# Kernel optimization log

Hardware: AMD Instinct MI355X
Metric: run time of the kernel (lower is better)

The kernel has to match this reference:

```python
import jax, jax.numpy as jnp
import numpy as np

HEADS = 8
HIDDEN = 512
SEQ = 1024
BATCH = 8
SCALE = 1.2
TOPK = round(0.05 * SEQ)  # 51, as in mode='stocastic'


def setup_inputs() -> dict:
    key = jax.random.key(0)
    ks = jax.random.split(key, 12)
    d = HIDDEN
    s = 0.02
    return {
        "Query_x": jax.random.normal(ks[0], (BATCH, SEQ, d), jnp.float32),
        "KeyandValue_x": jax.random.normal(ks[1], (BATCH, SEQ, d), jnp.float32),
        "Wq": jax.random.normal(ks[2], (d, d), jnp.float32) * s,
        "bq": jnp.zeros((d,), jnp.float32),
        "Wk": jax.random.normal(ks[3], (d, d), jnp.float32) * s,
        "bk": jnp.zeros((d,), jnp.float32),
        "Wv": jax.random.normal(ks[4], (d, d), jnp.float32) * s,
        "bv": jnp.zeros((d,), jnp.float32),
        "Wo": jax.random.normal(ks[5], (d, d), jnp.float32) * s,
        "bo": jnp.zeros((d,), jnp.float32),
        "randidx": jax.random.randint(ks[6], (round(0.1 * SEQ),), 0, SEQ, jnp.int32),
    }


def _split_heads(x, B, S):
    # torch: split last dim into heads chunks, cat along dim 0 -> [heads*B, S, dk]
    dk = HIDDEN // HEADS
    return x.reshape(B, S, HEADS, dk).transpose(2, 0, 1, 3).reshape(HEADS * B, S, dk)


def _merge_heads(x, B, S):
    dk = HIDDEN // HEADS
    return x.reshape(HEADS, B, S, dk).transpose(1, 2, 0, 3).reshape(B, S, HIDDEN)


def moderate_attention(a, randidx):
    # a: [N, S, L] softmaxed attention. Scale top-k + random columns by SCALE,
    # then renormalize rows. torch scatter_ writes a*SCALE gathered from the
    # pre-scatter tensor, so duplicate indices are idempotent -> boolean mask.
    N, S, L = a.shape
    _, idx = jax.lax.top_k(a, TOPK)                       # [N, S, k]
    rand_b = jnp.broadcast_to(randidx.astype(idx.dtype), (N, S, randidx.shape[0]))
    all_idx = jnp.concatenate([idx, rand_b], axis=-1)      # [N, S, k+r]
    n_ix = jnp.arange(N)[:, None, None]
    q_ix = jnp.arange(S)[None, :, None]
    sel = jnp.zeros(a.shape, bool).at[n_ix, q_ix, all_idx].set(True)
    a2 = jnp.where(sel, a * SCALE, a)
    return a2 / jnp.sum(a2, axis=-1, keepdims=True)


def reference(Query_x, KeyandValue_x, Wq, bq, Wk, bk, Wv, bv, Wo, bo, randidx):
    B, S, _ = Query_x.shape
    dk = HIDDEN // HEADS
    Q = _split_heads(Query_x @ Wq + bq, B, S)          # [H*B, S, dk]
    K = _split_heads(KeyandValue_x @ Wk + bk, B, S)
    V = _split_heads(KeyandValue_x @ Wv + bv, B, S)
    scores = jnp.einsum('nqd,nkd->nqk', Q, K) / jnp.sqrt(jnp.float32(dk))
    a = jax.nn.softmax(scores, axis=-1)
    a = moderate_attention(a, randidx)
    out = jnp.einsum('nqk,nkd->nqd', a, V)
    return _merge_heads(out, B, S) @ Wo + bo
```

## Files before the change

kernel.cpp:

```cpp
#include <hip/hip_runtime.h>
#include <stdint.h>

typedef unsigned short ushort_t;
typedef __bf16 bf16x8 __attribute__((ext_vector_type(8)));
typedef _Float16 f16x8v __attribute__((ext_vector_type(8)));
typedef __fp16 fp16x2 __attribute__((ext_vector_type(2)));
typedef float f32x4 __attribute__((ext_vector_type(4)));

#define SEQ   1024
#define DK    64
#define TOPK_N 51
#define RSCALE 1.2f
#define LOG2E    1.44269504089f
#define LOG2_12  0.26303440583f

#define OFF_WT  0
#define OFF_Q   (4*512*512)
#define OFF_K   (OFF_Q  + 64*1024*64)
#define OFF_V   (OFF_K  + 64*1024*64)
#define OFF_QX  (OFF_V  + 64*1024*64)
#define OFF_KVX (OFF_QX + 8192*512)
#define OFF_MASK (OFF_KVX + 8192*512)
#define OFF_A   OFF_QX

static __device__ __forceinline__ ushort_t f2bf(float f){
  union { float f; unsigned u; } x; x.f = f;
  unsigned r = x.u + 0x7FFFu + ((x.u >> 16) & 1u);
  return (ushort_t)(r >> 16);
}
static __device__ __forceinline__ ushort_t f2h(float f){
  union { _Float16 h; ushort_t u; } x; x.h = (_Float16)f; return x.u;
}
static __device__ __forceinline__ float h2f(ushort_t u){
  union { ushort_t u; _Float16 h; } x; x.u = u; return (float)x.h;
}
static __device__ __forceinline__ unsigned pk2(float a, float b){
  union { fp16x2 h; unsigned u; } x;
  x.h = __builtin_amdgcn_cvt_pkrtz(a, b);
  return x.u;
}
static __device__ __forceinline__ unsigned pkrne(float a, float b){
  return (unsigned)f2h(a) | ((unsigned)f2h(b) << 16);
}
static __device__ __forceinline__ bf16x8 frag16(const ushort_t* p){
  union { uint4 u; bf16x8 b; } x; x.u = *(const uint4*)p; return x.b;
}
static __device__ __forceinline__ f16x8v frag16h(const ushort_t* p){
  union { uint4 u; f16x8v h; } x; x.u = *(const uint4*)p; return x.h;
}
static __device__ __forceinline__ void gll16(const ushort_t* g, ushort_t* lds){
  __builtin_amdgcn_global_load_lds((const __attribute__((address_space(1))) unsigned*)g,
                                   (__attribute__((address_space(3))) unsigned*)lds,
                                   16, 0, 0);
}

__global__ __launch_bounds__(256) void prep_k(const float* qx, const float* kvx,
    const float* Wq, const float* Wk, const float* Wv, const float* Wo,
    const int* ridx, int nrand, ushort_t* ws){
  __shared__ ushort_t t[64][72];
  __shared__ unsigned wds[64];
  int bid = blockIdx.x, tid = threadIdx.x;

  if (bid < 4096){
    const float* src = (bid >= 2048) ? kvx : qx;
    ushort_t* dst = ws + ((bid >= 2048) ? OFF_KVX : OFF_QX);
    int i = ((bid & 2047)*256 + tid) * 8;
    float4 a = *(const float4*)(src + i);
    float4 b = *(const float4*)(src + i + 4);
    union { ushort_t s[8]; uint4 u; } p;
    p.s[0]=f2bf(a.x); p.s[1]=f2bf(a.y); p.s[2]=f2bf(a.z); p.s[3]=f2bf(a.w);
    p.s[4]=f2bf(b.x); p.s[5]=f2bf(b.y); p.s[6]=f2bf(b.z); p.s[7]=f2bf(b.w);
    *(uint4*)(dst + i) = p.u;
  } else if (bid < 4352){
    int rb = bid - 4096;
    int z = rb >> 6, rem = rb & 63;
    const float* W = z==0?Wq: z==1?Wk: z==2?Wv: Wo;
    ushort_t* O = ws + OFF_WT + (size_t)z*512*512;
    int kt = (rem >> 3)*64, nt = (rem & 7)*64;
    int r0 = tid>>3, c8 = (tid&7)*8;
    #pragma unroll
    for (int p=0;p<2;p++){
      int r = p*32 + r0;
      float4 a = *(const float4*)&W[(size_t)(kt+r)*512 + nt + c8];
      float4 b = *(const float4*)&W[(size_t)(kt+r)*512 + nt + c8 + 4];
      t[r][c8+0]=f2bf(a.x); t[r][c8+1]=f2bf(a.y); t[r][c8+2]=f2bf(a.z); t[r][c8+3]=f2bf(a.w);
      t[r][c8+4]=f2bf(b.x); t[r][c8+5]=f2bf(b.y); t[r][c8+6]=f2bf(b.z); t[r][c8+7]=f2bf(b.w);
    }
    __syncthreads();
    #pragma unroll
    for (int p=0;p<2;p++){
      int r = p*32 + r0;
      union { ushort_t s[8]; uint4 u; } tmp;
      #pragma unroll
      for (int j=0;j<8;j++) tmp.s[j] = t[c8+j][r];
      *(uint4*)&O[(size_t)(nt+r)*512 + kt + c8] = tmp.u;
    }
  } else {
    if (tid < 64) wds[tid] = 0;
    __syncthreads();
    for (int i = tid; i < nrand; i += 256){
      int col = ridx[i];
      atomicOr(&wds[(col >> 3) & 63], 1u << (((col >> 9) << 3) | (col & 7)));
    }
    __syncthreads();
    if (tid < 64) (ws + OFF_MASK)[tid] = (ushort_t)wds[tid];
  }
}

__global__ __launch_bounds__(256) void gemm_k(ushort_t* ws, const float* bq, const float* bk,
    const float* bv, const float* bo, float* dout, int base_mode){
  int mode = base_mode + blockIdx.z;
  const ushort_t* X  = (mode==0)? ws+OFF_QX : (mode==3)? ws+OFF_A : ws+OFF_KVX;
  const ushort_t* WT = ws + OFF_WT + (size_t)mode*(512*512);
  const float* bias  = (mode==0)?bq:(mode==1)?bk:(mode==2)?bv:bo;
  ushort_t* out = (mode==0)? ws+OFF_Q : (mode==1)? ws+OFF_K : ws+OFF_V;

  __shared__ ushort_t sA[128*64];
  __shared__ ushort_t sB[128*64];
  int tid = threadIdx.x, lane = tid & 63, w = tid >> 6;
  int wm = w & 1, wn = w >> 1;
  int m0 = blockIdx.y * 128, n0 = blockIdx.x * 128;
  int r16 = lane & 15, quad = lane >> 4;
  int srow = lane >> 3, schunk = lane & 7;

  const f32x4 zero = {0.f,0.f,0.f,0.f};
  f32x4 acc[4][4];
  #pragma unroll
  for (int i=0;i<4;i++)
    #pragma unroll
    for (int j=0;j<4;j++) acc[i][j] = zero;

  for (int kb = 0; kb < 8; kb++){
    int k0 = kb*64;
    #pragma unroll
    for (int i=0;i<4;i++){
      int rb = w*32 + i*8;
      int gch = schunk ^ srow;
      gll16(X  + (size_t)(m0+rb+srow)*512 + k0 + gch*8, sA + rb*64);
      gll16(WT + (size_t)(n0+rb+srow)*512 + k0 + gch*8, sB + rb*64);
    }
    __syncthreads();
    #pragma unroll
    for (int t=0;t<2;t++){
      bf16x8 aF[4], bF[4];
      #pragma unroll
      for (int i=0;i<4;i++){
        int row = wm*64 + i*16 + r16;
        aF[i] = frag16(sA + row*64 + ((t*4 + quad) ^ (row & 7))*8);
      }
      #pragma unroll
      for (int j=0;j<4;j++){
        int row = wn*64 + j*16 + r16;
        bF[j] = frag16(sB + row*64 + ((t*4 + quad) ^ (row & 7))*8);
      }
      #pragma unroll
      for (int i=0;i<4;i++)
        #pragma unroll
        for (int j=0;j<4;j++)
          acc[i][j] = __builtin_amdgcn_mfma_f32_16x16x32_bf16(aF[i], bF[j], acc[i][j], 0,0,0);
    }
    __syncthreads();
  }

  #pragma unroll
  for (int i=0;i<4;i++){
    int rowbase = m0 + wm*64 + i*16 + quad*4;
    #pragma unroll
    for (int j=0;j<4;j++){
      int col = n0 + wn*64 + j*16 + r16;
      float bsv = bias[col];
      if (mode == 3){
        #pragma unroll
        for (int r=0;r<4;r++)
          dout[(size_t)(rowbase+r)*512 + col] = acc[i][j][r] + bsv;
      } else if (mode == 2){
        int b = rowbase >> 10, s = rowbase & 1023;
        int h = col >> 6, d = col & 63;
        int nh = h*8 + b;
        union { ushort_t sh[4]; uint2 u2; } pk;
        #pragma unroll
        for (int r=0;r<4;r++) pk.sh[r] = f2h(acc[i][j][r] + bsv);
        *(uint2*)&out[ (((size_t)nh*128 + (s>>3))*64 + d)*8 + (s&4) ] = pk.u2;
      } else if (mode == 1){
        int b = rowbase >> 10;
        int h = col >> 6, d = col & 63;
        int nh = h*8 + b;
        size_t base = (size_t)nh*65536 + (size_t)(d>>3)*8192 + (d&7);
        #pragma unroll
        for (int r=0;r<4;r++){
          int s = (rowbase + r) & 1023;
          out[ base + (size_t)s*8 ] = f2bf(acc[i][j][r] + bsv);
        }
      } else {
        int h = col >> 6, d = col & 63;
        #pragma unroll
        for (int r=0;r<4;r++){
          int row = rowbase + r;
          int b = row >> 10, s = row & 1023;
          int nh = h*8 + b;
          out[ ((size_t)nh*1024 + s)*64 + d ] = f2bf((acc[i][j][r] + bsv)*0.125f);
        }
      }
    }
  }
}

__global__ __launch_bounds__(256, 4) void attn_k(const ushort_t* ws_q, const ushort_t* ws_k,
     const ushort_t* ws_v, const ushort_t* maskp, ushort_t* attn){
  __shared__ __align__(16) ushort_t sS[16*1024];

  int tid = threadIdx.x, lane = tid&63, w = tid>>6;
  int r16 = lane&15, quad = lane>>4;
  int gid = blockIdx.x;
  int n  = (gid & 7)*8 + ((gid >> 3) >> 6);
  int q0 = ((gid >> 3) & 63) * 16;
  const ushort_t* Qn = ws_q + (size_t)n*SEQ*DK;
  const ushort_t* Kn = ws_k + (size_t)n*SEQ*DK;
  const ushort_t* Vb = ws_v + (size_t)n*SEQ*DK;

  unsigned rmask = (unsigned)maskp[lane];

  bf16x8 aQ[2];
  #pragma unroll
  for (int t=0;t<2;t++)
    aQ[t] = frag16(Qn + (size_t)(q0 + r16)*64 + t*32 + quad*8);

  const f32x4 zero = {0.f,0.f,0.f,0.f};

  #pragma unroll
  for (int half=0; half<2; half++){
    f32x4 acc[8];
    #pragma unroll
    for (int i=0;i<8;i++) acc[i] = zero;
    #pragma unroll
    for (int grp=0; grp<2; grp++){
      int c = half*2 + grp;
      bf16x8 bF[8];
      #pragma unroll
      for (int u=0;u<4;u++){
        int key = c*256 + w*64 + u*16 + r16;
        bF[u*2+0] = frag16(Kn + ((size_t)(quad    )*1024 + key)*8);
        bF[u*2+1] = frag16(Kn + ((size_t)(4 + quad)*1024 + key)*8);
      }
      __builtin_amdgcn_s_setprio(1);
      #pragma unroll
      for (int u=0;u<4;u++){
        int t8 = grp*4 + u;
        acc[t8] = __builtin_amdgcn_mfma_f32_16x16x32_bf16(bF[u*2+0], aQ[0], acc[t8], 0,0,0);
        acc[t8] = __builtin_amdgcn_mfma_f32_16x16x32_bf16(bF[u*2+1], aQ[1], acc[t8], 0,0,0);
      }
      __builtin_amdgcn_s_setprio(0);
    }
    int rs = r16 & 7;
    #pragma unroll
    for (int grp=0; grp<2; grp++)
      #pragma unroll
      for (int u=0;u<4;u++){
        int kb = (half*2+grp)*256 + w*64 + u*16 + quad*4;
        f32x4 a = acc[grp*4+u];
        uint2 o;
        o.x = pkrne(a[0], a[1]);
        o.y = pkrne(a[2], a[3]);
        *(uint2*)(sS + r16*1024 + (((kb>>3) ^ rs) << 3) + (kb & 4)) = o;
      }
  }
  __syncthreads();

  float v[4][16];
  float vmax[4];
  #pragma unroll
  for (int r=0;r<4;r++){
    int row = w*4 + r, rs = row & 7;
    const ushort_t* bp = sS + row*1024 + ((lane ^ rs) * 8);
    uint4 lo4 = *(const uint4*)bp;
    uint4 hi4 = *(const uint4*)(bp + 512);
    unsigned wl[8] = {lo4.x, lo4.y, lo4.z, lo4.w, hi4.x, hi4.y, hi4.z, hi4.w};
    float m = -3.0e38f;
    #pragma unroll
    for (int k=0;k<8;k++){
      float a = h2f((ushort_t)(wl[k] & 0xffffu));
      float b = h2f((ushort_t)(wl[k] >> 16));
      v[r][2*k] = a; v[r][2*k+1] = b;
      m = fmaxf(m, fmaxf(a, b));
    }
    vmax[r] = m;
  }
  #pragma unroll
  for (int r=0;r<4;r++)
    #pragma unroll
    for (int j=0;j<16;j++)
      asm volatile("" : "+v"(v[r][j]));

  #pragma unroll
  for (int off=32; off>=1; off>>=1)
    #pragma unroll
    for (int r=0;r<4;r++) vmax[r] = fmaxf(vmax[r], __shfl_xor(vmax[r], off));

  float blo[4], bhi[4];
  #pragma unroll
  for (int r=0;r<4;r++){ bhi[r] = vmax[r]; blo[r] = vmax[r] - 4.0f; }
  #pragma unroll 1
  for (int it=0; it<11; it++){
    #pragma unroll
    for (int r=0;r<4;r++){
      float mid = 0.5f*(blo[r]+bhi[r]);
      int cnt = 0;
      #pragma unroll
      for (int j=0;j<16;j++)
        cnt += __popcll(__ballot(v[r][j] >= mid));
      bool ge = (cnt >= TOPK_N);
      blo[r] = ge ? mid : blo[r];
      bhi[r] = ge ? bhi[r] : mid;
    }
  }
  float fb[16];
  #pragma unroll
  for (int j=0;j<16;j++) fb[j] = ((rmask >> j) & 1u) ? LOG2_12 : 0.0f;
  float sC = LOG2_12;
  asm volatile("" : "+v"(sC));

  float ls[4];
  #pragma unroll
  for (int r=0;r<4;r++){
    float thr = blo[r], s = 0.f;
    #pragma unroll
    for (int j=0;j<16;j++){
      float tb = (v[r][j] >= thr) ? sC : fb[j];
      float e = __builtin_amdgcn_exp2f(
                  __builtin_fmaf(v[r][j] - vmax[r], LOG2E, tb));
      v[r][j] = e; s += e;
    }
    ls[r] = s;
  }
  #pragma unroll
  for (int off=32; off>=1; off>>=1)
    #pragma unroll
    for (int r=0;r<4;r++) ls[r] += __shfl_xor(ls[r], off);
  #pragma unroll
  for (int r=0;r<4;r++){
    int row = w*4 + r, rs = row & 7;
    float rinv = 1.0f / ls[r];
    ushort_t* bp = sS + row*1024 + ((lane ^ rs) * 8);
    uint4 o0, o1;
    o0.x = pk2(v[r][0]*rinv,  v[r][1]*rinv);
    o0.y = pk2(v[r][2]*rinv,  v[r][3]*rinv);
    o0.z = pk2(v[r][4]*rinv,  v[r][5]*rinv);
    o0.w = pk2(v[r][6]*rinv,  v[r][7]*rinv);
    o1.x = pk2(v[r][8]*rinv,  v[r][9]*rinv);
    o1.y = pk2(v[r][10]*rinv, v[r][11]*rinv);
    o1.z = pk2(v[r][12]*rinv, v[r][13]*rinv);
    o1.w = pk2(v[r][14]*rinv, v[r][15]*rinv);
    *(uint4*)bp = o0;
    *(uint4*)(bp + 512) = o1;
  }
  __syncthreads();

  f32x4 oa0 = zero, oa1 = zero;
  int dd = w*16 + r16;
  #pragma unroll
  for (int kb2=0; kb2<8; kb2++){
    f16x8v bV[4], aP[4];
    #pragma unroll
    for (int u=0;u<4;u++){
      int g8 = (kb2*4 + u)*4 + quad;
      bV[u] = frag16h(Vb + ((size_t)g8*64 + dd)*8);
      aP[u] = frag16h(sS + r16*1024 + ((g8 ^ (r16&7))*8));
    }
    __builtin_amdgcn_s_setprio(1);
    #pragma unroll
    for (int u=0;u<4;u++){
      if (u&1) oa1 = __builtin_amdgcn_mfma_f32_16x16x32_f16(aP[u], bV[u], oa1, 0,0,0);
      else     oa0 = __builtin_amdgcn_mfma_f32_16x16x32_f16(aP[u], bV[u], oa0, 0,0,0);
    }
    __builtin_amdgcn_s_setprio(0);
  }
  f32x4 oacc = oa0 + oa1;

  int h = n >> 3, b = n & 7;
  #pragma unroll
  for (int r=0;r<4;r++){
    int s = q0 + quad*4 + r;
    attn[ ((size_t)(b*1024 + s))*512 + h*64 + w*16 + r16 ] = f2bf(oacc[r]);
  }
}

extern "C" void kernel_launch(void* const* d_in, const int* in_sizes, int n_in,
                              void* d_out, int out_size, void* d_ws, size_t ws_size,
                              hipStream_t stream){
  const float* Qx  = (const float*)d_in[0];
  const float* KVx = (const float*)d_in[1];
  const float* Wq  = (const float*)d_in[2];
  const float* bq  = (const float*)d_in[3];
  const float* Wk  = (const float*)d_in[4];
  const float* bk  = (const float*)d_in[5];
  const float* Wv  = (const float*)d_in[6];
  const float* bv  = (const float*)d_in[7];
  const float* Wo  = (const float*)d_in[8];
  const float* bo  = (const float*)d_in[9];
  const int* ridx  = (const int*)d_in[10];
  int nrand = in_sizes[10];
  ushort_t* ws = (ushort_t*)d_ws;
  float* dout = (float*)d_out;

  prep_k<<<4353, 256, 0, stream>>>(Qx, KVx, Wq, Wk, Wv, Wo, ridx, nrand, ws);
  gemm_k<<<dim3(4,64,3), 256, 0, stream>>>(ws, bq, bk, bv, bo, dout, 0);
  attn_k<<<4096, 256, 0, stream>>>(ws+OFF_Q, ws+OFF_K, ws+OFF_V, ws+OFF_MASK, ws+OFF_A);
  gemm_k<<<dim3(4,64,1), 256, 0, stream>>>(ws, bq, bk, bv, bo, dout, 3);
}
```

Before: 234.9 us.

## Halve attention LDS score buffer and raise occupancy target to eight blocks

Shrinks the shared score tile from 16x1024 to 16x512 and streams the score row through it in two halves. Raw scores are held in registers between the halves, and probabilities are written back one half at a time for the PV matmul. Launch bounds now ask for eight blocks per CU instead of four, aiming to hide latency through higher occupancy. The cost is extra __syncthreads barriers and more live registers (raw and P0/P1 buffers), which may cause spills under the tighter register budget.

Measured after the change: 459.8 us. +95.7%, slower.

```diff
diff --git a/kernel.cpp b/kernel.cpp
--- a/kernel.cpp
+++ b/kernel.cpp
@@ -205,9 +205,9 @@
   }
 }
 
-__global__ __launch_bounds__(256, 4) void attn_k(const ushort_t* ws_q, const ushort_t* ws_k,
+__global__ __launch_bounds__(256, 8) void attn_k(const ushort_t* ws_q, const ushort_t* ws_k,
      const ushort_t* ws_v, const ushort_t* maskp, ushort_t* attn){
-  __shared__ __align__(16) ushort_t sS[16*1024];
+  __shared__ __align__(16) ushort_t sS[16*512];
 
   int tid = threadIdx.x, lane = tid&63, w = tid>>6;
   int r16 = lane&15, quad = lane>>4;
@@ -226,15 +226,17 @@
     aQ[t] = frag16(Qn + (size_t)(q0 + r16)*64 + t*32 + quad*8);
 
   const f32x4 zero = {0.f,0.f,0.f,0.f};
-
+  int myrow = w*4, rsr0 = myrow & 7;
+
+  uint4 raw[4][2];
   #pragma unroll
   for (int half=0; half<2; half++){
-    f32x4 acc[8];
-    #pragma unroll
-    for (int i=0;i<8;i++) acc[i] = zero;
     #pragma unroll
     for (int grp=0; grp<2; grp++){
       int c = half*2 + grp;
+      f32x4 acc[4];
+      #pragma unroll
+      for (int i=0;i<4;i++) acc[i] = zero;
       bf16x8 bF[8];
       #pragma unroll
       for (int u=0;u<4;u++){
@@ -245,43 +247,45 @@
       __builtin_amdgcn_s_setprio(1);
       #pragma unroll
       for (int u=0;u<4;u++){
-        int t8 = grp*4 + u;
-        acc[t8] = __builtin_amdgcn_mfma_f32_16x16x32_bf16(bF[u*2+0], aQ[0], acc[t8], 0,0,0);
-        acc[t8] = __builtin_amdgcn_mfma_f32_16x16x32_bf16(bF[u*2+1], aQ[1], acc[t8], 0,0,0);
+        acc[u] = __builtin_amdgcn_mfma_f32_16x16x32_bf16(bF[u*2+0], aQ[0], acc[u], 0,0,0);
+        acc[u] = __builtin_amdgcn_mfma_f32_16x16x32_bf16(bF[u*2+1], aQ[1], acc[u], 0,0,0);
       }
       __builtin_amdgcn_s_setprio(0);
-    }
-    int rs = r16 & 7;
-    #pragma unroll
-    for (int grp=0; grp<2; grp++)
+      int rs = r16 & 7;
       #pragma unroll
       for (int u=0;u<4;u++){
-        int kb = (half*2+grp)*256 + w*64 + u*16 + quad*4;
-        f32x4 a = acc[grp*4+u];
+        int kk = grp*256 + w*64 + u*16 + quad*4;
         uint2 o;
-        o.x = pkrne(a[0], a[1]);
-        o.y = pkrne(a[2], a[3]);
-        *(uint2*)(sS + r16*1024 + (((kb>>3) ^ rs) << 3) + (kb & 4)) = o;
-      }
-  }
-  __syncthreads();
+        o.x = pkrne(acc[u][0], acc[u][1]);
+        o.y = pkrne(acc[u][2], acc[u][3]);
+        *(uint2*)(sS + r16*512 + (((kk>>3) ^ rs) << 3) + (kk & 4)) = o;
+      }
+    }
+    __syncthreads();
+    #pragma unroll
+    for (int r=0;r<4;r++){
+      int row = myrow + r, rsr = row & 7;
+      raw[r][half] = *(const uint4*)(sS + row*512 + ((lane ^ rsr) * 8));
+    }
+    __syncthreads();
+  }
 
   float v[4][16];
   float vmax[4];
   #pragma unroll
   for (int r=0;r<4;r++){
-    int row = w*4 + r, rs = row & 7;
-    const ushort_t* bp = sS + row*1024 + ((lane ^ rs) * 8);
-    uint4 lo4 = *(const uint4*)bp;
-    uint4 hi4 = *(const uint4*)(bp + 512);
-    unsigned wl[8] = {lo4.x, lo4.y, lo4.z, lo4.w, hi4.x, hi4.y, hi4.z, hi4.w};
     float m = -3.0e38f;
     #pragma unroll
-    for (int k=0;k<8;k++){
-      float a = h2f((ushort_t)(wl[k] & 0xffffu));
-      float b = h2f((ushort_t)(wl[k] >> 16));
-      v[r][2*k] = a; v[r][2*k+1] = b;
-      m = fmaxf(m, fmaxf(a, b));
+    for (int half=0; half<2; half++){
+      unsigned wl[4] = {raw[r][half].x, raw[r][half].y, raw[r][half].z, raw[r][half].w};
+      #pragma unroll
+      for (int k=0;k<4;k++){
+        float a = h2f((ushort_t)(wl[k] & 0xffffu));
+        float b = h2f((ushort_t)(wl[k] >> 16));
+        v[r][half*8 + 2*k]     = a;
+        v[r][half*8 + 2*k + 1] = b;
+        m = fmaxf(m, fmaxf(a, b));
+      }
     }
     vmax[r] = m;
   }
@@ -336,35 +340,63 @@
   for (int off=32; off>=1; off>>=1)
     #pragma unroll
     for (int r=0;r<4;r++) ls[r] += __shfl_xor(ls[r], off);
-  #pragma unroll
-  for (int r=0;r<4;r++){
-    int row = w*4 + r, rs = row & 7;
+
+  uint4 P0[4], P1[4];
+  #pragma unroll
+  for (int r=0;r<4;r++){
     float rinv = 1.0f / ls[r];
-    ushort_t* bp = sS + row*1024 + ((lane ^ rs) * 8);
-    uint4 o0, o1;
-    o0.x = pk2(v[r][0]*rinv,  v[r][1]*rinv);
-    o0.y = pk2(v[r][2]*rinv,  v[r][3]*rinv);
-    o0.z = pk2(v[r][4]*rinv,  v[r][5]*rinv);
-    o0.w = pk2(v[r][6]*rinv,  v[r][7]*rinv);
-    o1.x = pk2(v[r][8]*rinv,  v[r][9]*rinv);
-    o1.y = pk2(v[r][10]*rinv, v[r][11]*rinv);
-    o1.z = pk2(v[r][12]*rinv, v[r][13]*rinv);
-    o1.w = pk2(v[r][14]*rinv, v[r][15]*rinv);
-    *(uint4*)bp = o0;
-    *(uint4*)(bp + 512) = o1;
-  }
-  __syncthreads();
+    P0[r].x = pk2(v[r][0]*rinv,  v[r][1]*rinv);
+    P0[r].y = pk2(v[r][2]*rinv,  v[r][3]*rinv);
+    P0[r].z = pk2(v[r][4]*rinv,  v[r][5]*rinv);
+    P0[r].w = pk2(v[r][6]*rinv,  v[r][7]*rinv);
+    P1[r].x = pk2(v[r][8]*rinv,  v[r][9]*rinv);
+    P1[r].y = pk2(v[r][10]*rinv, v[r][11]*rinv);
+    P1[r].z = pk2(v[r][12]*rinv, v[r][13]*rinv);
+    P1[r].w = pk2(v[r][14]*rinv, v[r][15]*rinv);
+  }
 
   f32x4 oa0 = zero, oa1 = zero;
   int dd = w*16 + r16;
-  #pragma unroll
-  for (int kb2=0; kb2<8; kb2++){
+  int rsA = r16 & 7;
+
+  #pragma unroll
+  for (int r=0;r<4;r++){
+    int row = myrow + r, rsr = row & 7;
+    *(uint4*)(sS + row*512 + ((lane ^ rsr) * 8)) = P0[r];
+  }
+  __syncthreads();
+  #pragma unroll
+  for (int kb2=0; kb2<4; kb2++){
     f16x8v bV[4], aP[4];
     #pragma unroll
     for (int u=0;u<4;u++){
       int g8 = (kb2*4 + u)*4 + quad;
       bV[u] = frag16h(Vb + ((size_t)g8*64 + dd)*8);
-      aP[u] = frag16h(sS + r16*1024 + ((g8 ^ (r16&7))*8));
+      aP[u] = frag16h(sS + r16*512 + ((g8 ^ rsA)*8));
+    }
+    __builtin_amdgcn_s_setprio(1);
+    #pragma unroll
+    for (int u=0;u<4;u++){
+      if (u&1) oa1 = __builtin_amdgcn_mfma_f32_16x16x32_f16(aP[u], bV[u], oa1, 0,0,0);
+      else     oa0 = __builtin_amdgcn_mfma_f32_16x16x32_f16(aP[u], bV[u], oa0, 0,0,0);
+    }
+    __builtin_amdgcn_s_setprio(0);
+  }
+  __syncthreads();
+  #pragma unroll
+  for (int r=0;r<4;r++){
+    int row = myrow + r, rsr = row & 7;
+    *(uint4*)(sS + row*512 + ((lane ^ rsr) * 8)) = P1[r];
+  }
+  __syncthreads();
+  #pragma unroll
+  for (int kb2=4; kb2<8; kb2++){
+    f16x8v bV[4], aP[4];
+    #pragma unroll
+    for (int u=0;u<4;u++){
+      int g8 = (kb2*4 + u)*4 + quad;
+      bV[u] = frag16h(Vb + ((size_t)g8*64 + dd)*8);
+      aP[u] = frag16h(sS + r16*512 + (((g8 & 63) ^ rsA)*8));
     }
     __builtin_amdgcn_s_setprio(1);
     #pragma unroll
```

## Double-buffer GEMM shared-memory tiles with K=32 stages to overlap loads

Applied to the files above, without the earlier changes.

Restructures the projection GEMM main loop to use two 128x32 shared-memory buffers per operand, prefetching the next K-slice via direct global-to-LDS loads while MFMAs consume the current one. The goal is to hide global load latency that the old single-buffered 64-wide K loop exposed at each barrier. The trade-off is twice as many iterations and barriers with a smaller per-stage tile, and the LDS swizzle changes to a 4-chunk XOR pattern, which may raise bank conflicts.

Result: no change. 231.1 us (-1.7%).

```diff
diff --git a/kernel.cpp b/kernel.cpp
--- a/kernel.cpp
+++ b/kernel.cpp
@@ -115,13 +115,13 @@
   const float* bias  = (mode==0)?bq:(mode==1)?bk:(mode==2)?bv:bo;
   ushort_t* out = (mode==0)? ws+OFF_Q : (mode==1)? ws+OFF_K : ws+OFF_V;
 
-  __shared__ ushort_t sA[128*64];
-  __shared__ ushort_t sB[128*64];
+  __shared__ ushort_t sA[2][128*32];
+  __shared__ ushort_t sB[2][128*32];
   int tid = threadIdx.x, lane = tid & 63, w = tid >> 6;
   int wm = w & 1, wn = w >> 1;
   int m0 = blockIdx.y * 128, n0 = blockIdx.x * 128;
   int r16 = lane & 15, quad = lane >> 4;
-  int srow = lane >> 3, schunk = lane & 7;
+  int srow = tid >> 2, sch = tid & 3;
 
   const f32x4 zero = {0.f,0.f,0.f,0.f};
   f32x4 acc[4][4];
@@ -130,37 +130,43 @@
     #pragma unroll
     for (int j=0;j<4;j++) acc[i][j] = zero;
 
-  for (int kb = 0; kb < 8; kb++){
-    int k0 = kb*64;
+  #define STAGE(t, buf)                                                        \
+    {                                                                          \
+      int k0 = (t)*32;                                                         \
+      _Pragma("unroll")                                                        \
+      for (int p=0;p<2;p++){                                                   \
+        int row = p*64 + srow;                                                 \
+        int gch = sch ^ (row & 3);                                             \
+        gll16(X  + (size_t)(m0+row)*512 + k0 + gch*8, &sA[buf][(p*64 + (w<<4))*32]); \
+        gll16(WT + (size_t)(n0+row)*512 + k0 + gch*8, &sB[buf][(p*64 + (w<<4))*32]); \
+      }                                                                        \
+    }
+
+  STAGE(0, 0);
+  __syncthreads();
+
+  for (int t = 0; t < 16; t++){
+    int buf = t & 1;
+    if (t < 15) STAGE(t+1, buf^1);
+    bf16x8 aF[4], bF[4];
     #pragma unroll
     for (int i=0;i<4;i++){
-      int rb = w*32 + i*8;
-      int gch = schunk ^ srow;
-      gll16(X  + (size_t)(m0+rb+srow)*512 + k0 + gch*8, sA + rb*64);
-      gll16(WT + (size_t)(n0+rb+srow)*512 + k0 + gch*8, sB + rb*64);
-    }
+      int row = wm*64 + i*16 + r16;
+      aF[i] = frag16(&sA[buf][row*32 + ((quad ^ (row & 3))*8)]);
+    }
+    #pragma unroll
+    for (int j=0;j<4;j++){
+      int row = wn*64 + j*16 + r16;
+      bF[j] = frag16(&sB[buf][row*32 + ((quad ^ (row & 3))*8)]);
+    }
+    #pragma unroll
+    for (int i=0;i<4;i++)
+      #pragma unroll
+      for (int j=0;j<4;j++)
+        acc[i][j] = __builtin_amdgcn_mfma_f32_16x16x32_bf16(aF[i], bF[j], acc[i][j], 0,0,0);
     __syncthreads();
-    #pragma unroll
-    for (int t=0;t<2;t++){
-      bf16x8 aF[4], bF[4];
-      #pragma unroll
-      for (int i=0;i<4;i++){
-        int row = wm*64 + i*16 + r16;
-        aF[i] = frag16(sA + row*64 + ((t*4 + quad) ^ (row & 7))*8);
-      }
-      #pragma unroll
-      for (int j=0;j<4;j++){
-        int row = wn*64 + j*16 + r16;
-        bF[j] = frag16(sB + row*64 + ((t*4 + quad) ^ (row & 7))*8);
-      }
-      #pragma unroll
-      for (int i=0;i<4;i++)
-        #pragma unroll
-        for (int j=0;j<4;j++)
-          acc[i][j] = __builtin_amdgcn_mfma_f32_16x16x32_bf16(aF[i], bF[j], acc[i][j], 0,0,0);
-    }
-    __syncthreads();
-  }
+  }
+  #undef STAGE
 
   #pragma unroll
   for (int i=0;i<4;i++){
```
